# Performance work log

Hardware: AMD Instinct MI355X
Metric: run time of the kernel (lower is better)

Reference implementation:

```python
import jax, jax.numpy as jnp
import numpy as np

NUM_HEAD = 16
NUM_SEQ = 2048
NUM_FEAT = 1024
HEAD_DIM = NUM_FEAT // NUM_HEAD
LN_EPS = 1e-5


def _constants():
    # decay per head: log(1 - 2^{-5-h})
    decay = jnp.log(1.0 - 2.0 ** (-5.0 - jnp.arange(NUM_HEAD, dtype=jnp.float32)))
    idx = jnp.arange(NUM_SEQ, dtype=jnp.float32)
    diff = idx[:, None] - idx[None, :]                      # [s, s]
    # exp(diff * decay) on lower triangle (incl. diagonal), 0 above
    mask = jnp.where(diff[None] >= 0, jnp.exp(diff[None] * decay[:, None, None]), 0.0)  # [h, s, s]
    # rotary angles: each frequency repeated twice
    angle = 1.0 / 10000.0 ** jnp.linspace(0.0, 1.0, HEAD_DIM // 2)
    angle = jnp.repeat(angle, 2)                            # [hd]
    sin = jnp.sin(idx[:, None] * angle[None, :])            # [s, hd]
    cos = jnp.cos(idx[:, None] * angle[None, :])
    return mask, sin, cos


def _rotate_every_two(x):
    x1 = x[..., ::2]
    x2 = x[..., 1::2]
    return jnp.stack((-x2, x1), axis=-1).reshape(x.shape)


def setup_inputs() -> dict:
    key = jax.random.key(0)
    ks = jax.random.split(key, 5)
    b, s, d = 4, NUM_SEQ, NUM_FEAT
    x = jax.random.normal(ks[0], (b, s, d), dtype=jnp.float32)
    Wq = jax.random.normal(ks[1], (d, d), dtype=jnp.float32) * 0.02
    Wk = jax.random.normal(ks[2], (d, d), dtype=jnp.float32) * 0.02
    Wv = jax.random.normal(ks[3], (d, d), dtype=jnp.float32) * 0.02
    Wo = jax.random.normal(ks[4], (d, d), dtype=jnp.float32) * 0.02
    ln_w = jnp.ones((HEAD_DIM,), dtype=jnp.float32)
    ln_b = jnp.zeros((HEAD_DIM,), dtype=jnp.float32)
    return {"x": x, "Wq": Wq, "Wk": Wk, "Wv": Wv, "Wo": Wo, "ln_w": ln_w, "ln_b": ln_b}


def reference(x, Wq, Wk, Wv, Wo, ln_w, ln_b):
    b, s, d = x.shape
    h, hd = NUM_HEAD, HEAD_DIM
    mask, sin, cos = _constants()

    def proj(W):
        # torch Linear (no bias): x @ W.T -> [b, h, s, hd]
        return (x @ W.T).reshape(b, s, h, hd).transpose(0, 2, 1, 3)

    q, k, v = proj(Wq), proj(Wk), proj(Wv)
    # rotary theta shift (sin/cos broadcast over batch & head)
    q = q * cos + _rotate_every_two(q) * sin
    k = k * cos + _rotate_every_two(k) * sin

    r = jnp.einsum('bhsd,bhtd->bhst', q, k) * mask[None]    # decay-masked scores
    o = jnp.einsum('bhst,bhtd->bhsd', r, v)                 # [b, h, s, hd]

    # LayerNorm over head_dim
    mu = jnp.mean(o, axis=-1, keepdims=True)
    var = jnp.var(o, axis=-1, keepdims=True)
    y = (o - mu) * jax.lax.rsqrt(var + LN_EPS) * ln_w + ln_b

    y = y.transpose(0, 2, 1, 3).reshape(b, s, d)
    return jax.nn.silu(y) @ Wo.T
```

## Files before the change

kernel.cpp:

```cpp
#include <hip/hip_runtime.h>
#include <math.h>

typedef unsigned short u16;
typedef __attribute__((ext_vector_type(8))) short short8;
typedef __attribute__((ext_vector_type(4))) float floatx4;

#define LDS_AS(p) ((__attribute__((address_space(3))) void*)(p))
#define GLB_AS(p) ((const __attribute__((address_space(1))) void*)(p))

__device__ __forceinline__ u16 f2bf(float f) {
  unsigned int u = __float_as_uint(f);
  u += 0x7fffu + ((u >> 16) & 1u);
  return (u16)(u >> 16);
}

__device__ __forceinline__ void gld16(const void* g, void* l) {
  __builtin_amdgcn_global_load_lds(GLB_AS(g), LDS_AS(l), 16, 0, 0);
}

__device__ __forceinline__ floatx4 mfma16(short8 a, short8 b, floatx4 c) {
  return __builtin_amdgcn_mfma_f32_16x16x32_bf16(a, b, c, 0, 0, 0);
}

__global__ void prep_kernel(const float* __restrict__ x, const float* __restrict__ Wq,
                            const float* __restrict__ Wk, const float* __restrict__ Wv,
                            const float* __restrict__ Wo, u16* __restrict__ xp,
                            u16* __restrict__ wqkvp, u16* __restrict__ wop,
                            float2* __restrict__ rtab) {
  int i = blockIdx.x * blockDim.x + threadIdx.x;
  const int str = gridDim.x * blockDim.x;
  for (; i < 3211264; i += str) {
    if (i < 3145728) {
      int U; u16* d;
      const float* s;
      if (i < 2097152)      { U = i;           d = xp;    s = x;  }
      else if (i < 2883584) { U = i - 2097152; d = wqkvp; s = nullptr; }
      else                  { U = i - 2883584; d = wop;   s = Wo; }
      const int tile = U >> 12;
      const int kc   = (U >> 7) & 31;
      const int lane = (U >> 1) & 63;
      const int jh   = U & 1;
      const int scol = kc * 32 + (lane >> 4) * 8 + jh * 4;
      int srow = tile * 16 + (lane & 15);
      if (s == nullptr) {
        const int sel = srow >> 10;
        srow &= 1023;
        s = (sel == 0) ? Wq : (sel == 1) ? Wk : Wv;
      }
      float4 v = ((const float4*)s)[srow * 256 + (scol >> 2)];
      ushort4 o;
      o.x = f2bf(v.x); o.y = f2bf(v.y); o.z = f2bf(v.z); o.w = f2bf(v.w);
      ((ushort4*)d)[U] = o;
    } else {
      const int t = i - 3145728;
      const int seq = t >> 5, dh = t & 31;
      const float freq = exp2f(-(float)dh * 0.42863594770f);
      float sn, cs;
      __sincosf((float)seq * freq, &sn, &cs);
      rtab[t] = make_float2(sn, cs);
    }
  }
}

template <int EPI>
__global__ __launch_bounds__(256, 2)
void gemm_bt(const u16* __restrict__ A, const u16* __restrict__ Bw, int K,
             u16* __restrict__ qb, u16* __restrict__ kb, u16* __restrict__ vtb,
             u16* __restrict__ kwt, const float2* __restrict__ rtab,
             float* __restrict__ outp) {
  constexpr int AP   = (EPI == 0) ? 8 : 4;
  constexpr int BUFU = (AP + 16) * 512;
  constexpr int AOFF = AP * 512;
  constexpr int AI   = (EPI == 0) ? 8 : 4;
  constexpr int IH   = (EPI == 0) ? 2 : 1;
  __shared__ __align__(16) u16 smem[3 * 12288];
  const int tid = threadIdx.x;
  const int w = tid >> 6, lane = tid & 63;
  const int quad = lane >> 4, l15 = lane & 15;
  const int m0 = blockIdx.y * (EPI == 0 ? 128 : 64), n0 = blockIdx.x * 256;

  const size_t tsz = (size_t)(K >> 5) * 512;
  const u16* A0 = A + ((size_t)(m0 >> 4) + (EPI == 0 ? 2 * w : w)) * tsz + lane * 8;
  const u16* A1 = A0 + tsz;
  const u16* Bb = Bw + ((size_t)(n0 >> 4) + 4 * w) * tsz + lane * 8;

  auto stage = [&](int buf, int kc) {
    const int nb = buf * BUFU;
    gld16(A0 + (size_t)kc * 512, &smem[nb + (EPI == 0 ? 2 * w : w) * 512]);
    if constexpr (EPI == 0)
      gld16(A1 + (size_t)kc * 512, &smem[nb + (2 * w + 1) * 512]);
#pragma unroll
    for (int e = 0; e < 4; ++e)
      gld16(Bb + (size_t)e * tsz + (size_t)kc * 512,
            &smem[nb + AOFF + (4 * w + e) * 512]);
  };

  floatx4 acc[AI][4] = {};
  const int NT = K >> 5;

  stage(0, 0);
  stage(1, 1);

  int cur = 0, stg = 2;
  for (int t = 0; t < NT; ++t) {
    if (t + 1 < NT) {
      if constexpr (EPI == 0)
        asm volatile("s_waitcnt vmcnt(6)" ::: "memory");
      else
        asm volatile("s_waitcnt vmcnt(5)" ::: "memory");
    } else {
      asm volatile("s_waitcnt vmcnt(0)" ::: "memory");
    }
    __builtin_amdgcn_s_barrier();
    asm volatile("" ::: "memory");
    __builtin_amdgcn_sched_barrier(0);

    if (t + 2 < NT) stage(stg, t + 2);

    const u16* Ap = &smem[cur * BUFU];
    const u16* Bp = Ap + AOFF;
    short8 a[AI], b[4];
#pragma unroll
    for (int i = 0; i < AI; ++i)
      a[i] = *(const short8*)&Ap[i * 512 + lane * 8];
#pragma unroll
    for (int j = 0; j < 4; ++j)
      b[j] = *(const short8*)&Bp[(w * 4 + j) * 512 + lane * 8];
    __builtin_amdgcn_s_setprio(1);
#pragma unroll
    for (int i = 0; i < AI; ++i)
#pragma unroll
      for (int j = 0; j < 4; ++j)
        acc[i][j] = mfma16(a[i], b[j], acc[i][j]);
    __builtin_amdgcn_s_setprio(0);
    asm volatile("" ::: "memory");
    cur = (cur == 2) ? 0 : cur + 1;
    stg = (stg == 2) ? 0 : stg + 1;
  }
  __builtin_amdgcn_s_barrier();

  u16* scr = &smem[w * 4096];

  const int ncb = n0 + w * 64;
  const int lr = lane >> 3, lc = lane & 7;

#pragma unroll
  for (int ih = 0; ih < IH; ++ih) {
    const int mrb = m0 + ih * 64;

    if (EPI == 0) {
      const int which = n0 >> 10;
      const int c1024 = ncb & 1023;
      const int bidx = mrb >> 11;
      const int hh = c1024 >> 6;
      const int seq0 = mrb & 2047;

      if (which < 2) {
#pragma unroll
        for (int j = 0; j < 4; ++j) {
          const int d = j * 16 + l15;
          const int dc = d >> 3, dl = d & 7;
#pragma unroll
          for (int i = 0; i < 4; ++i)
#pragma unroll
            for (int r = 0; r < 4; ++r) {
              const int sl = i * 16 + quad * 4 + r;
              const int seq = seq0 + sl;
              const float v = acc[ih * 4 + i][j][r];
              const float p = __shfl_xor(v, 1, 64);
              const float2 sc = rtab[(d >> 1) + seq * 32];
              const float res = (d & 1) ? (v * sc.y + p * sc.x) : (v * sc.y - p * sc.x);
              scr[sl * 64 + (((dc + (sl >> 2)) & 7) << 3) + dl] = f2bf(res);
            }
        }
        u16* dst = ((which == 0) ? qb : kb) + (size_t)(bidx * 16 + hh) * 131072 +
                   (size_t)seq0 * 64;
#pragma unroll
        for (int cch = 0; cch < 8; ++cch) {
          const int row = cch * 8 + lr;
          const int slot = (lc + (row >> 2)) & 7;
          short8 vv = *(const short8*)&scr[row * 64 + slot * 8];
          *(short8*)(dst + (size_t)row * 64 + lc * 8) = vv;
        }
        if (which == 1) {
          const float l2h = __log2f(1.0f - exp2f(-(float)(5 + hh)));
#pragma unroll
          for (int j = 0; j < 4; ++j) {
            const int d = j * 16 + l15;
#pragma unroll
            for (int i = 0; i < 4; ++i) {
              ushort4 pk;
#pragma unroll
              for (int r = 0; r < 4; ++r) {
                const int sl = i * 16 + quad * 4 + r;
                const int seq = seq0 + sl;
                const float v = acc[ih * 4 + i][j][r];
                const float p = __shfl_xor(v, 1, 64);
                const float2 sc = rtab[(d >> 1) + seq * 32];
                const float res = (d & 1) ? (v * sc.y + p * sc.x) : (v * sc.y - p * sc.x);
                const float wgt = exp2f((float)(127 - (seq & 127)) * l2h);
                ((u16*)&pk)[r] = f2bf(res * wgt);
              }
              *(ushort4*)&scr[d * 64 + ((i * 16 + quad * 4 + 8 * (d & 7)) & 63)] = pk;
            }
          }
          u16* dw = kwt + (size_t)(bidx * 16 + hh) * 131072 + seq0;
#pragma unroll
          for (int cch = 0; cch < 8; ++cch) {
            const int drow = cch * 8 + lr;
            const int slot = (lc + (drow & 7)) & 7;
            short8 vv = *(const short8*)&scr[drow * 64 + slot * 8];
            *(short8*)(dw + (size_t)drow * 2048 + lc * 8) = vv;
          }
        }
      } else {
#pragma unroll
        for (int j = 0; j < 4; ++j) {
          const int d = j * 16 + l15;
#pragma unroll
          for (int i = 0; i < 4; ++i) {
            ushort4 pk;
            pk.x = f2bf(acc[ih * 4 + i][j][0]);
            pk.y = f2bf(acc[ih * 4 + i][j][1]);
            pk.z = f2bf(acc[ih * 4 + i][j][2]);
            pk.w = f2bf(acc[ih * 4 + i][j][3]);
            *(ushort4*)&scr[d * 64 + ((i * 16 + quad * 4 + 8 * (d & 7)) & 63)] = pk;
          }
        }
        u16* dh = vtb + (size_t)(bidx * 16 + hh) * 131072 + seq0;
#pragma unroll
        for (int cch = 0; cch < 8; ++cch) {
          const int drow = cch * 8 + lr;
          const int slot = (lc + (drow & 7)) & 7;
          short8 vv = *(const short8*)&scr[drow * 64 + slot * 8];
          *(short8*)(dh + (size_t)drow * 2048 + lc * 8) = vv;
        }
      }
    } else {
      float* scrf = (float*)scr;
      const int lr4 = lane >> 4, lc16 = lane & 15;
#pragma unroll
      for (int p = 0; p < 4; ++p) {
#pragma unroll
        for (int j = 0; j < 4; ++j)
#pragma unroll
          for (int r = 0; r < 4; ++r)
            scrf[(quad * 4 + r) * 65 + j * 16 + l15] = acc[p][j][r];
#pragma unroll
        for (int cch = 0; cch < 4; ++cch) {
          const int rr = cch * 4 + lr4;
          float4 vv = *(const float4*)&scrf[rr * 65 + lc16 * 4];
          *(float4*)&outp[(size_t)(mrb + p * 16 + rr) * 1024 + ncb + lc16 * 4] = vv;
        }
      }
    }
  }
}

__global__ __launch_bounds__(256, 4)
void kvchunk_kernel(const u16* __restrict__ kwt, const u16* __restrict__ vtb,
                    float* __restrict__ U) {
  __shared__ __align__(16) u16 kls[16 * 512];
  __shared__ __align__(16) u16 vls[16 * 512];
  const int c = blockIdx.x, bh = blockIdx.y;
  const int tid = threadIdx.x, w = tid >> 6, lane = tid & 63;
  const int quad = lane >> 4, l15 = lane & 15;
  const u16* kg = kwt + (size_t)bh * 131072 + c * 128;
  const u16* vg = vtb + (size_t)bh * 131072 + c * 128;
#pragma unroll
  for (int rg = 0; rg < 4; ++rg) {
    const int rid = w * 4 + rg;
    const int m = rid >> 2, kst = rid & 3;
    gld16(kg + (size_t)(m * 16 + l15) * 2048 + kst * 32 + quad * 8, &kls[rid * 512]);
    gld16(vg + (size_t)(m * 16 + l15) * 2048 + kst * 32 + quad * 8, &vls[rid * 512]);
  }
  __syncthreads();
  floatx4 acc[4] = {};
#pragma unroll
  for (int kst = 0; kst < 4; ++kst) {
    short8 bf = *(const short8*)&vls[(w * 4 + kst) * 512 + lane * 8];
#pragma unroll
    for (int m = 0; m < 4; ++m) {
      short8 af = *(const short8*)&kls[(m * 4 + kst) * 512 + lane * 8];
      acc[m] = mfma16(af, bf, acc[m]);
    }
  }
  float* Ub = U + ((size_t)bh * 16 + c) * 4096;
#pragma unroll
  for (int m = 0; m < 4; ++m)
#pragma unroll
    for (int r = 0; r < 4; ++r)
      Ub[(m * 16 + quad * 4 + r) * 64 + w * 16 + l15] = acc[m][r];
}

__global__ void scan_kernel(const float* __restrict__ U, u16* __restrict__ Sb) {
  const int bh = blockIdx.x;
  const int w = threadIdx.x >> 6, l = threadIdx.x & 63;
  const int h = bh & 15;
  const float l2 = __log2f(1.0f - exp2f(-(float)(5 + h)));
  const float lamL = exp2f(128.0f * l2);
  float S[16];
#pragma unroll
  for (int i = 0; i < 16; ++i) S[i] = 0.f;
  for (int c = 0; c < 16; ++c) {
    u16* sp = Sb + ((size_t)bh * 16 + c) * 4096 + l * 64 + w * 16;
#pragma unroll
    for (int dk = 0; dk < 16; dk += 4) {
      ushort4 pk;
      pk.x = f2bf(S[dk]);     pk.y = f2bf(S[dk + 1]);
      pk.z = f2bf(S[dk + 2]); pk.w = f2bf(S[dk + 3]);
      *(ushort4*)&sp[dk] = pk;
    }
    const float* up = U + ((size_t)bh * 16 + c) * 4096 + (w * 16) * 64 + l;
#pragma unroll
    for (int dk = 0; dk < 16; ++dk)
      S[dk] = lamL * S[dk] + up[dk * 64];
  }
}

__global__ __launch_bounds__(256, 2)
void attn_chunk_kernel(const u16* __restrict__ qb, const u16* __restrict__ kb,
                       const u16* __restrict__ vtb, const u16* __restrict__ Sb,
                       const float* __restrict__ lnw, const float* __restrict__ lnb,
                       u16* __restrict__ yb) {
  __shared__ __align__(16) u16 kls[16 * 512];
  __shared__ __align__(16) u16 vls[16 * 512];
  __shared__ __align__(16) u16 Sls[8 * 512];
  __shared__ __align__(16) u16 pls[4 * 32 * 40];

  const int c = blockIdx.x, bh = blockIdx.y, h = bh & 15;
  const int tid = threadIdx.x;
  const int w = tid >> 6, lane = tid & 63, quad = lane >> 4, l15 = lane & 15;
  const float l2 = __log2f(1.0f - exp2f(-(float)(5 + h)));

  const u16* kg = kb + (size_t)bh * 131072 + (size_t)c * 128 * 64;
  const u16* vg = vtb + (size_t)bh * 131072 + (size_t)c * 128;
  const u16* Sg = Sb + ((size_t)bh * 16 + c) * 4096;
#pragma unroll
  for (int rg = 0; rg < 4; ++rg) {
    const int kid = w * 4 + rg;
    const int nsub = kid >> 1, kk = kid & 1;
    gld16(kg + (size_t)(nsub * 16 + l15) * 64 + kk * 32 + quad * 8, &kls[kid * 512]);
    const int jd = kid >> 2, kst = kid & 3;
    gld16(vg + (size_t)(jd * 16 + l15) * 2048 + kst * 32 + quad * 8, &vls[kid * 512]);
  }
#pragma unroll
  for (int e = 0; e < 2; ++e) {
    const int rid = w * 2 + e;
    const int nd = rid >> 1, kk = rid & 1;
    gld16(Sg + (size_t)(nd * 16 + l15) * 64 + kk * 32 + quad * 8, &Sls[rid * 512]);
  }

  short8 qf[2][2];
  {
    const u16* qbase = qb + ((size_t)bh * 2048 + c * 128 + w * 32 + l15) * 64 + quad * 8;
#pragma unroll
    for (int i = 0; i < 2; ++i)
#pragma unroll
      for (int kk = 0; kk < 2; ++kk)
        qf[i][kk] = *(const short8*)(qbase + (size_t)i * 16 * 64 + kk * 32);
  }
  float lnwv[4], lnbv[4];
#pragma unroll
  for (int jd = 0; jd < 4; ++jd) {
    lnwv[jd] = lnw[jd * 16 + l15];
    lnbv[jd] = lnb[jd * 16 + l15];
  }
  __syncthreads();

  floatx4 sacc[2][8] = {};
#pragma unroll
  for (int kk = 0; kk < 2; ++kk) {
    short8 bf[8];
#pragma unroll
    for (int j = 0; j < 8; ++j)
      bf[j] = *(const short8*)&kls[(j * 2 + kk) * 512 + lane * 8];
#pragma unroll
    for (int i = 0; i < 2; ++i)
#pragma unroll
      for (int j = 0; j < 8; ++j)
        sacc[i][j] = mfma16(qf[i][kk], bf[j], sacc[i][j]);
  }

  floatx4 oacc[2][4] = {};
#pragma unroll
  for (int kk = 0; kk < 2; ++kk)
#pragma unroll
    for (int nd = 0; nd < 4; ++nd) {
      short8 sf = *(const short8*)&Sls[(nd * 2 + kk) * 512 + lane * 8];
#pragma unroll
      for (int i = 0; i < 2; ++i)
        oacc[i][nd] = mfma16(qf[i][kk], sf, oacc[i][nd]);
    }
  float rowf[8];
#pragma unroll
  for (int i = 0; i < 2; ++i)
#pragma unroll
    for (int r = 0; r < 4; ++r)
      rowf[i * 4 + r] = exp2f((float)(w * 32 + i * 16 + quad * 4 + r) * l2);
  const float lam1 = exp2f(l2);
#pragma unroll
  for (int i = 0; i < 2; ++i)
#pragma unroll
    for (int nd = 0; nd < 4; ++nd)
#pragma unroll
      for (int r = 0; r < 4; ++r)
        oacc[i][nd][r] *= rowf[i * 4 + r] * lam1;

  float colf[8];
#pragma unroll
  for (int j = 0; j < 8; ++j) colf[j] = exp2f(-(float)(j * 16 + l15) * l2);
  u16* pw = &pls[w * 1280];
#pragma unroll
  for (int kst = 0; kst < 4; ++kst) {
#pragma unroll
    for (int jl = 0; jl < 2; ++jl) {
      const int j = kst * 2 + jl;
#pragma unroll
      for (int i = 0; i < 2; ++i)
#pragma unroll
        for (int r = 0; r < 4; ++r) {
          const int srow = i * 16 + quad * 4 + r;
          const int dlt = (w * 32 + srow) - (j * 16 + l15);
          const float v =
              (dlt >= 0) ? sacc[i][j][r] * rowf[i * 4 + r] * colf[j] : 0.0f;
          pw[srow * 40 + jl * 16 + l15] = f2bf(v);
        }
    }
    short8 pf[2], vf[4];
#pragma unroll
    for (int i = 0; i < 2; ++i)
      pf[i] = *(const short8*)&pw[(i * 16 + l15) * 40 + quad * 8];
#pragma unroll
    for (int jd = 0; jd < 4; ++jd)
      vf[jd] = *(const short8*)&vls[(jd * 4 + kst) * 512 + lane * 8];
#pragma unroll
    for (int i = 0; i < 2; ++i)
#pragma unroll
      for (int jd = 0; jd < 4; ++jd)
        oacc[i][jd] = mfma16(pf[i], vf[jd], oacc[i][jd]);
  }

  __syncthreads();
  u16* scrw = &kls[w * 2048];
  const int b = bh >> 4;
#pragma unroll
  for (int i = 0; i < 2; ++i)
#pragma unroll
    for (int r = 0; r < 4; ++r) {
      float sum = 0.f, ssq = 0.f;
#pragma unroll
      for (int jd = 0; jd < 4; ++jd) {
        const float v = oacc[i][jd][r];
        sum += v;
        ssq += v * v;
      }
#pragma unroll
      for (int off = 1; off < 16; off <<= 1) {
        sum += __shfl_xor(sum, off, 64);
        ssq += __shfl_xor(ssq, off, 64);
      }
      const float mu = sum * (1.0f / 64.0f);
      const float var = ssq * (1.0f / 64.0f) - mu * mu;
      const float rst = rsqrtf(var + 1e-5f);
      const int sl = i * 16 + quad * 4 + r;
#pragma unroll
      for (int jd = 0; jd < 4; ++jd) {
        const float z = (oacc[i][jd][r] - mu) * rst * lnwv[jd] + lnbv[jd];
        const float y = z / (1.0f + expf(-z));
        const int f = jd * 16 + l15;
        scrw[sl * 64 + ((((f >> 3) + (sl >> 2)) & 7) << 3) + (f & 7)] = f2bf(y);
      }
    }
  const int tile0 = b * 128 + c * 8 + w * 2;
#pragma unroll
  for (int tt = 0; tt < 2; ++tt)
#pragma unroll
    for (int kcl = 0; kcl < 2; ++kcl) {
      const int row = tt * 16 + l15;
      const int slot = ((kcl * 4 + quad) + (row >> 2)) & 7;
      short8 vv = *(const short8*)&scrw[row * 64 + slot * 8];
      *(short8*)(yb + ((size_t)(tile0 + tt) * 32 + h * 2 + kcl) * 512 + lane * 8) = vv;
    }
}

extern "C" void kernel_launch(void* const* d_in, const int* in_sizes, int n_in,
                              void* d_out, int out_size, void* d_ws, size_t ws_size,
                              hipStream_t stream) {
  const float* x   = (const float*)d_in[0];
  const float* Wq  = (const float*)d_in[1];
  const float* Wk  = (const float*)d_in[2];
  const float* Wv  = (const float*)d_in[3];
  const float* Wo  = (const float*)d_in[4];
  const float* lnw = (const float*)d_in[5];
  const float* lnb = (const float*)d_in[6];
  float* out = (float*)d_out;

  char* ws = (char*)d_ws;
  u16* xbf  = (u16*)(ws + 0);
  u16* wqkv = (u16*)(ws + 16777216);
  u16* Sb   = (u16*)(ws + 16777216);
  u16* qbuf = (u16*)(ws + 25165824);
  u16* kbuf = (u16*)(ws + 41943040);
  u16* vtb  = (u16*)(ws + 58720256);
  u16* wo   = (u16*)(ws + 75497472);
  float2* rtab = (float2*)(ws + 77594624);
  u16* yb   = xbf;
  u16* kwt  = (u16*)d_out;
  float* Ubuf = (float*)((char*)d_out + 16777216);

  prep_kernel<<<dim3(1024), dim3(256), 0, stream>>>(x, Wq, Wk, Wv, Wo, xbf, wqkv, wo,
                                                    rtab);
  gemm_bt<0><<<dim3(12, 64), dim3(256), 0, stream>>>(xbf, wqkv, 1024, qbuf, kbuf, vtb,
                                                     kwt, rtab, nullptr);
  kvchunk_kernel<<<dim3(16, 64), dim3(256), 0, stream>>>(kwt, vtb, Ubuf);
  scan_kernel<<<dim3(64), dim3(256), 0, stream>>>(Ubuf, Sb);
  attn_chunk_kernel<<<dim3(16, 64), dim3(256), 0, stream>>>(qbuf, kbuf, vtb, Sb, lnw,
                                                            lnb, yb);
  gemm_bt<1><<<dim3(4, 128), dim3(256), 0, stream>>>(yb, wo, 1024, nullptr, nullptr,
                                                     nullptr, nullptr, nullptr, out);
}
```

Measured before the change: 243.8 us.

## Store Q/K/V/S intermediates in MFMA-fragment-packed chunk layout for contiguous loads

The projection epilogue and scan kernel now write q, k, decayed kT, vT and the chunk state S in a per-chunk, fragment-ordered layout, so each 512-element MFMA operand tile is contiguous. The consumer kernels (kvchunk, attn_chunk) then issue fully contiguous global-to-LDS and register loads instead of strided row gathers. This removes strided, poorly coalesced reads, especially the 2048-stride transposed reads, at the cost of more complex producer-side LDS shuffling and a tight coupling between producer and consumer layouts.

```diff
diff --git a/kernel.cpp b/kernel.cpp
--- a/kernel.cpp
+++ b/kernel.cpp
@@ -21,6 +21,7 @@
 __device__ __forceinline__ floatx4 mfma16(short8 a, short8 b, floatx4 c) {
   return __builtin_amdgcn_mfma_f32_16x16x32_bf16(a, b, c, 0, 0, 0);
 }
+
 
 __global__ void prep_kernel(const float* __restrict__ x, const float* __restrict__ Wq,
                             const float* __restrict__ Wk, const float* __restrict__ Wv,
@@ -142,7 +143,6 @@
   u16* scr = &smem[w * 4096];
 
   const int ncb = n0 + w * 64;
-  const int lr = lane >> 3, lc = lane & 7;
 
 #pragma unroll
   for (int ih = 0; ih < IH; ++ih) {
@@ -154,6 +154,7 @@
       const int bidx = mrb >> 11;
       const int hh = c1024 >> 6;
       const int seq0 = mrb & 2047;
+      const int chk = seq0 >> 7;
 
       if (which < 2) {
 #pragma unroll
@@ -173,15 +174,17 @@
               scr[sl * 64 + (((dc + (sl >> 2)) & 7) << 3) + dl] = f2bf(res);
             }
         }
-        u16* dst = ((which == 0) ? qb : kb) + (size_t)(bidx * 16 + hh) * 131072 +
-                   (size_t)seq0 * 64;
-#pragma unroll
-        for (int cch = 0; cch < 8; ++cch) {
-          const int row = cch * 8 + lr;
-          const int slot = (lc + (row >> 2)) & 7;
-          short8 vv = *(const short8*)&scr[row * 64 + slot * 8];
-          *(short8*)(dst + (size_t)row * 64 + lc * 8) = vv;
-        }
+        u16* dst = ((which == 0) ? qb : kb) +
+                   (((size_t)(bidx * 16 + hh) * 16 + chk) << 13);
+#pragma unroll
+        for (int nl = 0; nl < 4; ++nl)
+#pragma unroll
+          for (int kk2 = 0; kk2 < 2; ++kk2) {
+            const int slr = nl * 16 + l15;
+            const int slot = ((kk2 * 4 + quad) + (slr >> 2)) & 7;
+            short8 vv = *(const short8*)&scr[slr * 64 + slot * 8];
+            *(short8*)(dst + (((ih * 4 + nl) * 2 + kk2) * 512) + lane * 8) = vv;
+          }
         if (which == 1) {
           const float l2h = __log2f(1.0f - exp2f(-(float)(5 + hh)));
 #pragma unroll
@@ -204,14 +207,16 @@
               *(ushort4*)&scr[d * 64 + ((i * 16 + quad * 4 + 8 * (d & 7)) & 63)] = pk;
             }
           }
-          u16* dw = kwt + (size_t)(bidx * 16 + hh) * 131072 + seq0;
-#pragma unroll
-          for (int cch = 0; cch < 8; ++cch) {
-            const int drow = cch * 8 + lr;
-            const int slot = (lc + (drow & 7)) & 7;
-            short8 vv = *(const short8*)&scr[drow * 64 + slot * 8];
-            *(short8*)(dw + (size_t)drow * 2048 + lc * 8) = vv;
-          }
+          u16* dw = kwt + (((size_t)(bidx * 16 + hh) * 16 + chk) << 13);
+#pragma unroll
+          for (int m = 0; m < 4; ++m)
+#pragma unroll
+            for (int ks2 = 0; ks2 < 2; ++ks2) {
+              const int dr = m * 16 + l15;
+              const int col = ((ks2 * 32 + quad * 8) + 8 * (dr & 7)) & 63;
+              short8 vv = *(const short8*)&scr[dr * 64 + col];
+              *(short8*)(dw + ((m * 4 + ih * 2 + ks2) * 512) + lane * 8) = vv;
+            }
         }
       } else {
 #pragma unroll
@@ -227,14 +232,16 @@
             *(ushort4*)&scr[d * 64 + ((i * 16 + quad * 4 + 8 * (d & 7)) & 63)] = pk;
           }
         }
-        u16* dh = vtb + (size_t)(bidx * 16 + hh) * 131072 + seq0;
-#pragma unroll
-        for (int cch = 0; cch < 8; ++cch) {
-          const int drow = cch * 8 + lr;
-          const int slot = (lc + (drow & 7)) & 7;
-          short8 vv = *(const short8*)&scr[drow * 64 + slot * 8];
-          *(short8*)(dh + (size_t)drow * 2048 + lc * 8) = vv;
-        }
+        u16* dh = vtb + (((size_t)(bidx * 16 + hh) * 16 + chk) << 13);
+#pragma unroll
+        for (int m = 0; m < 4; ++m)
+#pragma unroll
+          for (int ks2 = 0; ks2 < 2; ++ks2) {
+            const int dr = m * 16 + l15;
+            const int col = ((ks2 * 32 + quad * 8) + 8 * (dr & 7)) & 63;
+            short8 vv = *(const short8*)&scr[dr * 64 + col];
+            *(short8*)(dh + ((m * 4 + ih * 2 + ks2) * 512) + lane * 8) = vv;
+          }
       }
     } else {
       float* scrf = (float*)scr;
@@ -265,14 +272,13 @@
   const int c = blockIdx.x, bh = blockIdx.y;
   const int tid = threadIdx.x, w = tid >> 6, lane = tid & 63;
   const int quad = lane >> 4, l15 = lane & 15;
-  const u16* kg = kwt + (size_t)bh * 131072 + c * 128;
-  const u16* vg = vtb + (size_t)bh * 131072 + c * 128;
+  const u16* kg = kwt + (((size_t)bh * 16 + c) << 13);
+  const u16* vg = vtb + (((size_t)bh * 16 + c) << 13);
 #pragma unroll
   for (int rg = 0; rg < 4; ++rg) {
     const int rid = w * 4 + rg;
-    const int m = rid >> 2, kst = rid & 3;
-    gld16(kg + (size_t)(m * 16 + l15) * 2048 + kst * 32 + quad * 8, &kls[rid * 512]);
-    gld16(vg + (size_t)(m * 16 + l15) * 2048 + kst * 32 + quad * 8, &vls[rid * 512]);
+    gld16(kg + rid * 512 + lane * 8, &kls[rid * 512]);
+    gld16(vg + rid * 512 + lane * 8, &vls[rid * 512]);
   }
   __syncthreads();
   floatx4 acc[4] = {};
@@ -303,13 +309,14 @@
 #pragma unroll
   for (int i = 0; i < 16; ++i) S[i] = 0.f;
   for (int c = 0; c < 16; ++c) {
-    u16* sp = Sb + ((size_t)bh * 16 + c) * 4096 + l * 64 + w * 16;
-#pragma unroll
-    for (int dk = 0; dk < 16; dk += 4) {
-      ushort4 pk;
-      pk.x = f2bf(S[dk]);     pk.y = f2bf(S[dk + 1]);
-      pk.z = f2bf(S[dk + 2]); pk.w = f2bf(S[dk + 3]);
-      *(ushort4*)&sp[dk] = pk;
+    u16* sp = Sb + (((size_t)bh * 16 + c) << 12);
+#pragma unroll
+    for (int g = 0; g < 2; ++g) {
+      short8 pk;
+#pragma unroll
+      for (int j = 0; j < 8; ++j) ((u16*)&pk)[j] = f2bf(S[g * 8 + j]);
+      const int lp = ((w & 1) * 2 + g) * 16 + (l & 15);
+      *(short8*)(sp + (((l >> 4) * 2 + (w >> 1)) * 512) + lp * 8) = pk;
     }
     const float* up = U + ((size_t)bh * 16 + c) * 4096 + (w * 16) * 64 + l;
 #pragma unroll
@@ -333,32 +340,29 @@
   const int w = tid >> 6, lane = tid & 63, quad = lane >> 4, l15 = lane & 15;
   const float l2 = __log2f(1.0f - exp2f(-(float)(5 + h)));
 
-  const u16* kg = kb + (size_t)bh * 131072 + (size_t)c * 128 * 64;
-  const u16* vg = vtb + (size_t)bh * 131072 + (size_t)c * 128;
-  const u16* Sg = Sb + ((size_t)bh * 16 + c) * 4096;
+  const u16* kg = kb + (((size_t)bh * 16 + c) << 13);
+  const u16* vg = vtb + (((size_t)bh * 16 + c) << 13);
+  const u16* Sg = Sb + (((size_t)bh * 16 + c) << 12);
 #pragma unroll
   for (int rg = 0; rg < 4; ++rg) {
     const int kid = w * 4 + rg;
-    const int nsub = kid >> 1, kk = kid & 1;
-    gld16(kg + (size_t)(nsub * 16 + l15) * 64 + kk * 32 + quad * 8, &kls[kid * 512]);
-    const int jd = kid >> 2, kst = kid & 3;
-    gld16(vg + (size_t)(jd * 16 + l15) * 2048 + kst * 32 + quad * 8, &vls[kid * 512]);
+    gld16(kg + kid * 512 + lane * 8, &kls[kid * 512]);
+    gld16(vg + kid * 512 + lane * 8, &vls[kid * 512]);
   }
 #pragma unroll
   for (int e = 0; e < 2; ++e) {
     const int rid = w * 2 + e;
-    const int nd = rid >> 1, kk = rid & 1;
-    gld16(Sg + (size_t)(nd * 16 + l15) * 64 + kk * 32 + quad * 8, &Sls[rid * 512]);
+    gld16(Sg + rid * 512 + lane * 8, &Sls[rid * 512]);
   }
 
   short8 qf[2][2];
   {
-    const u16* qbase = qb + ((size_t)bh * 2048 + c * 128 + w * 32 + l15) * 64 + quad * 8;
+    const u16* qp = qb + (((size_t)bh * 16 + c) << 13);
 #pragma unroll
     for (int i = 0; i < 2; ++i)
 #pragma unroll
       for (int kk = 0; kk < 2; ++kk)
-        qf[i][kk] = *(const short8*)(qbase + (size_t)i * 16 * 64 + kk * 32);
+        qf[i][kk] = *(const short8*)(qp + (((w * 2 + i) * 2 + kk) * 512) + lane * 8);
   }
   float lnwv[4], lnbv[4];
 #pragma unroll
```

Result: no change. 239.2 us (-1.9%).
